# Kernel tuning notes

Hardware: AMD Instinct MI355X
Metric: run time of the kernel (lower is better)

The kernel has to match this reference:

```python
import jax, jax.numpy as jnp
import numpy as np

EPS = 1e-5


def setup_inputs() -> dict:
    key = jax.random.key(0)
    k0, k1, k2, k3 = jax.random.split(key, 4)
    B, C, H, W = 64, 128, 64, 64
    x = jax.random.normal(k0, (B, C, H, W), dtype=jnp.float32)
    w = jax.random.normal(k1, (C, C, 1), dtype=jnp.float32) * 0.05  # conv1d kernel_size=1 weight
    b = jax.random.normal(k2, (C,), dtype=jnp.float32) * 0.05       # conv1d bias
    s = jax.random.normal(k3, (1, C, 1), dtype=jnp.float32)         # learned per-channel gate logits
    offset = jnp.ones((1,), dtype=jnp.float32) * 8.0                 # module inits offset to 8
    return {"x": x, "w": w, "b": b, "s": s, "offset": offset}


def reference(x, w, b, s, offset):
    B, C, H, W = x.shape
    HW = H * W
    # Checkerboard mask: mask[c, l] = (c + l) % 2  (even channel -> [0,1,0,1,...])
    c_idx = jnp.arange(C)
    l_idx = jnp.arange(HW)
    mask = ((c_idx[:, None] + l_idx[None, :]) % 2).astype(x.dtype)  # (C, HW)

    x_flat = x.reshape(B, C, HW)
    x_masked = x_flat * mask                                         # (B, C, HW)
    # 1x1 conv1d: pointwise channel mix + bias
    z = jnp.einsum('oc,bcl->bol', w[:, :, 0], x_masked) + b[None, :, None]
    pool = z.mean(axis=1)                                            # avgpool over channels -> (B, HW)
    g = jax.nn.sigmoid(pool + offset) + EPS                          # (B, HW)
    s_sig = jax.nn.sigmoid(s[0, :, 0]) + EPS                         # (C,)

    attn_mask = (1.0 - mask)[None] * g[:, None, :] + mask[None] * s_sig[None, :, None]  # (B,C,HW)
    out = x * attn_mask.reshape(B, C, H, W)

    logdet = (C // 2) * jnp.sum(jnp.log(g), axis=-1)                 # (B,)
    logdet = logdet + B * jnp.sum(jnp.log(s_sig)[:, None] * mask)    # scalar broadcast over batch
    return out, logdet
```

## Files before the change

kernel.cpp:

```cpp
#include <hip/hip_runtime.h>
#include <hip/hip_bf16.h>
#include <math.h>


#define EPS 1e-5f
#define NC 128
#define NHW 4096
#define NB 64
#define LT 64
#define NLT (NHW / LT)

typedef __attribute__((ext_vector_type(4))) float f4;


__global__ __launch_bounds__(256) void prep_kernel(const float* __restrict__ w,
                                                   const float* __restrict__ bias,
                                                   const float* __restrict__ s,
                                                   float* __restrict__ ws,
                                                   float* __restrict__ logdet) {
    __shared__ float wpart[256];
    __shared__ float lred[NC];
    __shared__ float bred[NC];
    __shared__ float ldconst;

    const int tid = threadIdx.x;
    {
        const int c  = tid & 127;
        const int o0 = (tid >> 7) * 64;
        const float* __restrict__ wp = w + (size_t)o0 * NC + c;
        float a0 = 0.f, a1 = 0.f, a2 = 0.f, a3 = 0.f;
        float a4 = 0.f, a5 = 0.f, a6 = 0.f, a7 = 0.f;
#pragma unroll
        for (int o = 0; o < 64; o += 8) {
            a0 += wp[(o + 0) * NC];
            a1 += wp[(o + 1) * NC];
            a2 += wp[(o + 2) * NC];
            a3 += wp[(o + 3) * NC];
            a4 += wp[(o + 4) * NC];
            a5 += wp[(o + 5) * NC];
            a6 += wp[(o + 6) * NC];
            a7 += wp[(o + 7) * NC];
        }
        wpart[tid] = (((a0 + a1) + (a2 + a3)) + ((a4 + a5) + (a6 + a7)));
    }
    __syncthreads();

    if (tid < NC) {
        ws[tid] = (wpart[tid] + wpart[NC + tid]) * (1.f / NC);
        const float ssig = 1.f / (1.f + expf(-s[tid])) + EPS;
        ws[NC + tid] = ssig;
        lred[tid] = logf(ssig);
        bred[tid] = bias[tid];
    }
    __syncthreads();

    if (tid == 0) {
        double sb = 0.0, sl = 0.0;
        for (int i = 0; i < NC; ++i) { sb += (double)bred[i]; sl += (double)lred[i]; }
        ws[256] = (float)(sb / NC);
        ldconst = (float)((double)NB * (double)(NHW / 2) * sl);
    }
    __syncthreads();
    if (tid < NB) logdet[tid] = ldconst;
}

__global__ __launch_bounds__(256) void main_kernel(const float* __restrict__ x,
                                                   const float* __restrict__ ws,
                                                   const float* __restrict__ offp,
                                                   float* __restrict__ out,
                                                   float* __restrict__ logdet) {
    __shared__ float4 pp[4][16];

    const int tid  = threadIdx.x;
    const int j    = tid & 15;
    const int cg   = tid >> 4;
    const int wave = tid >> 6;
    const int lane = tid & 63;

    const int lt = blockIdx.x;
    const int b  = blockIdx.y;
    const int l0 = lt * LT;

    const size_t base = (size_t)b * (NC * NHW) + (size_t)(cg * 8) * NHW + l0 + j * 4;
    const float* __restrict__ xp = x + base;

    float4 v[8];
#pragma unroll
    for (int k = 0; k < 8; ++k)
        v[k] = *reinterpret_cast<const float4*>(xp + (size_t)k * NHW);

    float4 acc = make_float4(0.f, 0.f, 0.f, 0.f);
#pragma unroll
    for (int k = 0; k < 8; ++k) {
        const int c = cg * 8 + k;
        const float wb = ws[c];
        if (c & 1) { acc.x += wb * v[k].x; acc.z += wb * v[k].z; }
        else       { acc.y += wb * v[k].y; acc.w += wb * v[k].w; }
    }

#pragma unroll
    for (int off = 16; off <= 32; off <<= 1) {
        acc.x += __shfl_xor(acc.x, off);
        acc.y += __shfl_xor(acc.y, off);
        acc.z += __shfl_xor(acc.z, off);
        acc.w += __shfl_xor(acc.w, off);
    }
    if (lane < 16) pp[wave][j] = acc;
    __syncthreads();

    const float4 p0 = pp[0][j], p1 = pp[1][j], p2 = pp[2][j], p3 = pp[3][j];
    const float cst = ws[256] + offp[0];
    float4 g;
    g.x = 1.f / (1.f + __expf(-(p0.x + p1.x + p2.x + p3.x + cst))) + EPS;
    g.y = 1.f / (1.f + __expf(-(p0.y + p1.y + p2.y + p3.y + cst))) + EPS;
    g.z = 1.f / (1.f + __expf(-(p0.z + p1.z + p2.z + p3.z + cst))) + EPS;
    g.w = 1.f / (1.f + __expf(-(p0.w + p1.w + p2.w + p3.w + cst))) + EPS;

    if (wave == 0) {
        float slg = (lane < 16)
                  ? (__logf(g.x) + __logf(g.y) + __logf(g.z) + __logf(g.w))
                  : 0.f;
#pragma unroll
        for (int off = 32; off > 0; off >>= 1) slg += __shfl_down(slg, off);
        if (lane == 0) atomicAdd(&logdet[b], 64.f * slg);
    }

    const float* __restrict__ ssig = ws + NC;
    float* __restrict__ op = out + base;
#pragma unroll
    for (int k = 0; k < 8; ++k) {
        const int c = cg * 8 + k;
        const float sc = ssig[c];
        f4 o;
        if (c & 1) { o.x = v[k].x * sc;  o.y = v[k].y * g.y;
                     o.z = v[k].z * sc;  o.w = v[k].w * g.w; }
        else       { o.x = v[k].x * g.x; o.y = v[k].y * sc;
                     o.z = v[k].z * g.z; o.w = v[k].w * sc; }
        __builtin_nontemporal_store(o, reinterpret_cast<f4*>(op + (size_t)k * NHW));
    }
}

extern "C" void kernel_launch(void* const* d_in, const int* in_sizes, int n_in,
                              void* d_out, int out_size, void* d_ws, size_t ws_size,
                              hipStream_t stream) {
    const float* x    = (const float*)d_in[0];
    const float* w    = (const float*)d_in[1];
    const float* bias = (const float*)d_in[2];
    const float* s    = (const float*)d_in[3];
    const float* offp = (const float*)d_in[4];

    float* out    = (float*)d_out;
    float* logdet = out + (size_t)NB * NC * NHW;
    float* ws     = (float*)d_ws;

    prep_kernel<<<1, 256, 0, stream>>>(w, bias, s, ws, logdet);
    main_kernel<<<dim3(NLT, NB), 256, 0, stream>>>(x, ws, offp, out, logdet);
}
```

Baseline: 58.93 us.

## Widen spatial tile to 1024-thread blocks and replace atomics with partials reduction

Each block now covers 256 spatial positions with 1024 threads (16 channel groups of 8), reducing the channel sum through a larger shared-memory array instead of cross-lane shuffles. The per-batch logdet atomicAdd is replaced by writing per-tile partials to workspace, which a new small finalize kernel reduces and adds to the constant term. This cuts the block count and removes atomic contention, at the cost of an extra kernel launch, a heavier block-wide barrier, and possibly lower occupancy flexibility.

```diff
diff --git a/kernel.cpp b/kernel.cpp
--- a/kernel.cpp
+++ b/kernel.cpp
@@ -7,7 +7,7 @@
 #define NC 128
 #define NHW 4096
 #define NB 64
-#define LT 64
+#define LT 256
 #define NLT (NHW / LT)
 
 typedef __attribute__((ext_vector_type(4))) float f4;
@@ -16,12 +16,10 @@
 __global__ __launch_bounds__(256) void prep_kernel(const float* __restrict__ w,
                                                    const float* __restrict__ bias,
                                                    const float* __restrict__ s,
-                                                   float* __restrict__ ws,
-                                                   float* __restrict__ logdet) {
+                                                   float* __restrict__ ws) {
     __shared__ float wpart[256];
     __shared__ float lred[NC];
     __shared__ float bred[NC];
-    __shared__ float ldconst;
 
     const int tid = threadIdx.x;
     {
@@ -58,24 +56,20 @@
         double sb = 0.0, sl = 0.0;
         for (int i = 0; i < NC; ++i) { sb += (double)bred[i]; sl += (double)lred[i]; }
         ws[256] = (float)(sb / NC);
-        ldconst = (float)((double)NB * (double)(NHW / 2) * sl);
+        ws[257] = (float)((double)NB * (double)(NHW / 2) * sl);
     }
-    __syncthreads();
-    if (tid < NB) logdet[tid] = ldconst;
 }
 
-__global__ __launch_bounds__(256) void main_kernel(const float* __restrict__ x,
-                                                   const float* __restrict__ ws,
-                                                   const float* __restrict__ offp,
-                                                   float* __restrict__ out,
-                                                   float* __restrict__ logdet) {
-    __shared__ float4 pp[4][16];
+__global__ __launch_bounds__(1024) void main_kernel(const float* __restrict__ x,
+                                                    const float* __restrict__ ws,
+                                                    const float* __restrict__ offp,
+                                                    float* __restrict__ out,
+                                                    float* __restrict__ partials) {
+    __shared__ float4 pp[16][64];
 
     const int tid  = threadIdx.x;
-    const int j    = tid & 15;
-    const int cg   = tid >> 4;
-    const int wave = tid >> 6;
-    const int lane = tid & 63;
+    const int j    = tid & 63;
+    const int cg   = tid >> 6;
 
     const int lt = blockIdx.x;
     const int b  = blockIdx.y;
@@ -98,31 +92,27 @@
         else       { acc.y += wb * v[k].y; acc.w += wb * v[k].w; }
     }
 
-#pragma unroll
-    for (int off = 16; off <= 32; off <<= 1) {
-        acc.x += __shfl_xor(acc.x, off);
-        acc.y += __shfl_xor(acc.y, off);
-        acc.z += __shfl_xor(acc.z, off);
-        acc.w += __shfl_xor(acc.w, off);
-    }
-    if (lane < 16) pp[wave][j] = acc;
+    pp[cg][j] = acc;
     __syncthreads();
 
-    const float4 p0 = pp[0][j], p1 = pp[1][j], p2 = pp[2][j], p3 = pp[3][j];
+    float4 p = pp[0][j];
+#pragma unroll
+    for (int wv = 1; wv < 16; ++wv) {
+        const float4 q = pp[wv][j];
+        p.x += q.x; p.y += q.y; p.z += q.z; p.w += q.w;
+    }
     const float cst = ws[256] + offp[0];
     float4 g;
-    g.x = 1.f / (1.f + __expf(-(p0.x + p1.x + p2.x + p3.x + cst))) + EPS;
-    g.y = 1.f / (1.f + __expf(-(p0.y + p1.y + p2.y + p3.y + cst))) + EPS;
-    g.z = 1.f / (1.f + __expf(-(p0.z + p1.z + p2.z + p3.z + cst))) + EPS;
-    g.w = 1.f / (1.f + __expf(-(p0.w + p1.w + p2.w + p3.w + cst))) + EPS;
+    g.x = 1.f / (1.f + __expf(-(p.x + cst))) + EPS;
+    g.y = 1.f / (1.f + __expf(-(p.y + cst))) + EPS;
+    g.z = 1.f / (1.f + __expf(-(p.z + cst))) + EPS;
+    g.w = 1.f / (1.f + __expf(-(p.w + cst))) + EPS;
 
-    if (wave == 0) {
-        float slg = (lane < 16)
-                  ? (__logf(g.x) + __logf(g.y) + __logf(g.z) + __logf(g.w))
-                  : 0.f;
+    if (cg == 0) {
+        float slg = __logf(g.x) + __logf(g.y) + __logf(g.z) + __logf(g.w);
 #pragma unroll
         for (int off = 32; off > 0; off >>= 1) slg += __shfl_down(slg, off);
-        if (lane == 0) atomicAdd(&logdet[b], 64.f * slg);
+        if (j == 0) partials[b * NLT + lt] = slg;
     }
 
     const float* __restrict__ ssig = ws + NC;
@@ -140,6 +130,18 @@
     }
 }
 
+__global__ __launch_bounds__(64) void fin_kernel(const float* __restrict__ partials,
+                                                 const float* __restrict__ ws,
+                                                 float* __restrict__ logdet,
+                                                 int nlt) {
+    const int b = blockIdx.x;
+    const int t = threadIdx.x;
+    float v = (t < nlt) ? partials[b * nlt + t] : 0.f;
+#pragma unroll
+    for (int off = 32; off > 0; off >>= 1) v += __shfl_down(v, off);
+    if (t == 0) logdet[b] = 64.f * v + ws[257];
+}
+
 extern "C" void kernel_launch(void* const* d_in, const int* in_sizes, int n_in,
                               void* d_out, int out_size, void* d_ws, size_t ws_size,
                               hipStream_t stream) {
@@ -152,7 +154,9 @@
     float* out    = (float*)d_out;
     float* logdet = out + (size_t)NB * NC * NHW;
     float* ws     = (float*)d_ws;
+    float* partials = ws + 512;
 
-    prep_kernel<<<1, 256, 0, stream>>>(w, bias, s, ws, logdet);
-    main_kernel<<<dim3(NLT, NB), 256, 0, stream>>>(x, ws, offp, out, logdet);
+    prep_kernel<<<1, 256, 0, stream>>>(w, bias, s, ws);
+    main_kernel<<<dim3(NLT, NB), 1024, 0, stream>>>(x, ws, offp, out, partials);
+    fin_kernel<<<NB, 64, 0, stream>>>(partials, ws, logdet, NLT);
 }
```

New measurement: 59.07 us. About the same (+0.2%).
